# Kernel tuning notes

Hardware: AMD Instinct MI355X
Metric: run time of the kernel (lower is better)

Reference implementation:

```python
import jax, jax.numpy as jnp
import numpy as np
from jax import lax

DIM = 256
STATE = 64
D_INNER = 256          # ssd_expand=1 * dim
HIDDEN = 4 * DIM       # mlp_ratio=4
CONV_DIM = 3 * STATE
B, H, W = 16, 64, 64
EPS = 1e-5


def dwconv(x, w, b=None):
    # depthwise 3x3, SAME padding; x:(B,C,H,W) w:(C,1,3,3)
    y = lax.conv_general_dilated(x, w, (1, 1), 'SAME',
                                 feature_group_count=x.shape[1],
                                 dimension_numbers=('NCHW', 'OIHW', 'NCHW'))
    if b is not None:
        y = y + b[None, :, None, None]
    return y


def batchnorm(x, g, b):
    m = x.mean(axis=(0, 2, 3), keepdims=True)
    v = x.var(axis=(0, 2, 3), keepdims=True)
    return (x - m) * jax.lax.rsqrt(v + EPS) * g[None, :, None, None] + b[None, :, None, None]


def layernorm1d(x, w, b):
    # norm over channel dim of (B,C,L)
    m = x.mean(axis=1, keepdims=True)
    v = x.var(axis=1, keepdims=True)
    return (x - m) * jax.lax.rsqrt(v + EPS) * w[None, :, None] + b[None, :, None]


def pw1d(x, w, b):
    # 1x1 conv1d: x:(B,Cin,L), w:(Cout,Cin)
    return jnp.einsum('oc,bcl->bol', w, x) + b[None, :, None]


def setup_inputs() -> dict:
    key = jax.random.key(0)
    ks = jax.random.split(key, 16)
    s = 0.02
    inp = {
        'x': jax.random.normal(ks[0], (B, DIM, H, W), jnp.float32),
        'alpha': 1e-4 * jnp.ones((4, DIM), jnp.float32),
        'dw1_w': s * jax.random.normal(ks[1], (DIM, 1, 3, 3), jnp.float32),
        'bn1_g': jnp.ones((DIM,), jnp.float32),
        'bn1_b': jnp.zeros((DIM,), jnp.float32),
        'dw2_w': s * jax.random.normal(ks[2], (DIM, 1, 3, 3), jnp.float32),
        'bn2_g': jnp.ones((DIM,), jnp.float32),
        'bn2_b': jnp.zeros((DIM,), jnp.float32),
        'ln_w': jnp.ones((DIM,), jnp.float32),
        'ln_b': jnp.zeros((DIM,), jnp.float32),
        'bcdt_w': s * jax.random.normal(ks[3], (CONV_DIM, DIM), jnp.float32),
        'bcdt_b': jnp.zeros((CONV_DIM,), jnp.float32),
        'mdw_w': s * jax.random.normal(ks[4], (CONV_DIM, 1, 3, 3), jnp.float32),
        'mdw_b': jnp.zeros((CONV_DIM,), jnp.float32),
        'hz_w': s * jax.random.normal(ks[5], (2 * D_INNER, DIM), jnp.float32),
        'hz_b': jnp.zeros((2 * D_INNER,), jnp.float32),
        'out_w': s * jax.random.normal(ks[6], (DIM, D_INNER), jnp.float32),
        'out_b': jnp.zeros((DIM,), jnp.float32),
        'A': jax.random.uniform(ks[7], (STATE,), jnp.float32, 1.0, 16.0),
        'D': jnp.ones((1,), jnp.float32),
        'ffn_w1': s * jax.random.normal(ks[8], (HIDDEN, DIM), jnp.float32),
        'ffn_b1': jnp.zeros((HIDDEN,), jnp.float32),
        'ffn_w2': s * jax.random.normal(ks[9], (DIM, HIDDEN), jnp.float32),
        'ffn_b2': jnp.zeros((DIM,), jnp.float32),
    }
    return inp


def _mixer(xf, bcdt_w, bcdt_b, mdw_w, mdw_b, hz_w, hz_b, out_w, out_b, A, D, h_, w_):
    # xf: (B, dim, L)
    b = xf.shape[0]
    BCdt = pw1d(xf, bcdt_w, bcdt_b).reshape(b, CONV_DIM, h_, w_)
    BCdt = dwconv(BCdt, mdw_w, mdw_b).reshape(b, CONV_DIM, h_ * w_)
    Bm, Cm, dt = jnp.split(BCdt, [STATE, 2 * STATE], axis=1)  # (B,S,L) each
    Am = jax.nn.softmax(dt + A[None, :, None], axis=-1)
    AB = Am * Bm                                   # (B,S,L)
    h = jnp.einsum('bcl,bsl->bcs', xf, AB)         # (B,dim,S) small
    hz = jnp.einsum('oc,bcs->bos', hz_w, h) + hz_b[None, :, None]
    hh, z = jnp.split(hz, [D_INNER], axis=1)
    hh = hh * jax.nn.silu(z) + hh * D[0]
    hh = jnp.einsum('oc,bcs->bos', out_w, hh) + out_b[None, :, None]
    y = jnp.einsum('bcs,bsl->bcl', hh, Cm)         # (B,dim,L)
    return y.reshape(b, DIM, h_, w_)


def reference(x, alpha, dw1_w, bn1_g, bn1_b, dw2_w, bn2_g, bn2_b, ln_w, ln_b,
              bcdt_w, bcdt_b, mdw_w, mdw_b, hz_w, hz_b, out_w, out_b, A, D,
              ffn_w1, ffn_b1, ffn_w2, ffn_b2):
    a = jax.nn.sigmoid(alpha)[:, None, :, None, None]  # (4,1,dim,1,1)
    x = (1 - a[0]) * x + a[0] * batchnorm(dwconv(x, dw1_w), bn1_g, bn1_b)
    x_prev = x
    b, _, h_, w_ = x.shape
    xf = layernorm1d(x.reshape(b, DIM, h_ * w_), ln_w, ln_b)
    y = _mixer(xf, bcdt_w, bcdt_b, mdw_w, mdw_b, hz_w, hz_b, out_w, out_b, A, D, h_, w_)
    x = (1 - a[1]) * x_prev + a[1] * y
    x = (1 - a[2]) * x + a[2] * batchnorm(dwconv(x, dw2_w), bn2_g, bn2_b)
    # FFN: 1x1 conv -> GELU -> 1x1 conv
    hdn = jax.nn.gelu(jnp.einsum('oc,bchw->bohw', ffn_w1, x) + ffn_b1[None, :, None, None])
    x_ffn = jnp.einsum('oc,bchw->bohw', ffn_w2, hdn) + ffn_b2[None, :, None, None]
    x = (1 - a[3]) * x + a[3] * x_ffn
    return x
```

## Files before the change

### kernel.cpp

```cpp
#include <hip/hip_runtime.h>
#include <stdint.h>


typedef __attribute__((ext_vector_type(8))) short bf16x8;
typedef __attribute__((ext_vector_type(4))) float f32x4;

__device__ __forceinline__ unsigned short f2b(float f){
  union { float f; unsigned int u; } v; v.f = f;
  unsigned int r = v.u + 0x7FFFu + ((v.u >> 16) & 1u);
  return (unsigned short)(r >> 16);
}
__device__ __forceinline__ float b2f(unsigned short h){
  union { unsigned int u; float f; } v; v.u = ((unsigned int)h) << 16;
  return v.f;
}
__device__ __forceinline__ float sigm(float x){ return 1.0f / (1.0f + __expf(-x)); }
__device__ __forceinline__ float gelu_fast(float v){
  float t = v * (-2.3022059f - 0.10294886f * v * v);
  float e = __builtin_amdgcn_exp2f(t);
  return v * __builtin_amdgcn_rcpf(1.0f + e);
}
__device__ __forceinline__ unsigned int cvtpk(float lo, float hi){
  unsigned int r;
  asm volatile("v_cvt_pk_bf16_f32 %0, %1, %2" : "=v"(r) : "v"(lo), "v"(hi));
  return r;
}
__device__ __forceinline__ f32x4 mfma16(bf16x8 a, bf16x8 b, f32x4 c){
  return __builtin_amdgcn_mfma_f32_16x16x32_bf16(a, b, c, 0, 0, 0);
}
__device__ __forceinline__ bf16x8 ldb8g(const unsigned short* p){
  return *reinterpret_cast<const bf16x8*>(p);
}
__device__ __forceinline__ f32x4 zero4(){ f32x4 v = {0.f, 0.f, 0.f, 0.f}; return v; }
__device__ __forceinline__ void gload_lds16(const unsigned short* g, unsigned short* l){
  __builtin_amdgcn_global_load_lds(
      (const __attribute__((address_space(1))) void*)g,
      (__attribute__((address_space(3))) void*)l, 16, 0, 0);
}

__global__ __launch_bounds__(256) void k_setup(
    const float* __restrict__ w1, const float* __restrict__ w2,
    const float* __restrict__ bw, const float* __restrict__ hzw,
    const float* __restrict__ outw,
    unsigned short* __restrict__ w1b, unsigned short* __restrict__ w2b,
    unsigned short* __restrict__ bwb, unsigned short* __restrict__ hzwb,
    unsigned short* __restrict__ outwb){
  int tid = blockIdx.x * 256 + threadIdx.x;
  if (tid < 1024 * 256){ w1b[tid] = f2b(w1[tid]); w2b[tid] = f2b(w2[tid]); }
  if (tid < 192 * 256)  bwb[tid] = f2b(bw[tid]);
  if (tid < 512 * 256)  hzwb[tid] = f2b(hzw[tid]);
  if (tid < 256 * 256)  outwb[tid] = f2b(outw[tid]);
}

__global__ __launch_bounds__(256) void k_conv_stats(
    const float* __restrict__ x, const float* __restrict__ w,
    float* __restrict__ bnsum, float* __restrict__ bnsq){
  __shared__ float t[66 * 66];
  __shared__ float rs[4], rq[4];
  int bc = blockIdx.x; int c = bc & 255;
  const float* xp = x + (size_t)bc * 4096;
  int tid = threadIdx.x;
  for (int i = tid; i < 66 * 66; i += 256) t[i] = 0.f;
  __syncthreads();
  #pragma unroll
  for (int j = 0; j < 4; j++){
    int p4 = tid + j * 256;
    float4 v = reinterpret_cast<const float4*>(xp)[p4];
    int p = p4 * 4; int y = p >> 6, xx = p & 63;
    int base = (y + 1) * 66 + xx + 1;
    t[base] = v.x; t[base + 1] = v.y; t[base + 2] = v.z; t[base + 3] = v.w;
  }
  __syncthreads();
  float w0 = w[c*9+0], w1 = w[c*9+1], w2 = w[c*9+2], w3 = w[c*9+3], w4 = w[c*9+4];
  float w5 = w[c*9+5], w6 = w[c*9+6], w7 = w[c*9+7], w8 = w[c*9+8];
  float s = 0.f, q = 0.f;
  #pragma unroll
  for (int j = 0; j < 16; j++){
    int p = tid + j * 256; int y = p >> 6, xx = p & 63;
    const float* r0 = &t[y * 66 + xx];
    float v = r0[0]*w0 + r0[1]*w1 + r0[2]*w2 + r0[66]*w3 + r0[67]*w4 + r0[68]*w5
            + r0[132]*w6 + r0[133]*w7 + r0[134]*w8;
    s += v; q += v * v;
  }
  #pragma unroll
  for (int off = 32; off > 0; off >>= 1){ s += __shfl_down(s, off); q += __shfl_down(q, off); }
  if ((tid & 63) == 0){ rs[tid >> 6] = s; rq[tid >> 6] = q; }
  __syncthreads();
  if (tid == 0){
    atomicAdd(&bnsum[c], rs[0] + rs[1] + rs[2] + rs[3]);
    atomicAdd(&bnsq[c],  rq[0] + rq[1] + rq[2] + rq[3]);
  }
}

__global__ __launch_bounds__(256) void k_conv_bn_blend(
    const float* __restrict__ x, const float* __restrict__ w,
    const float* __restrict__ bnsum, const float* __restrict__ bnsq,
    const float* __restrict__ g, const float* __restrict__ bb,
    const float* __restrict__ alpha, float* __restrict__ out){
  __shared__ float t[66 * 66];
  int bc = blockIdx.x; int c = bc & 255;
  const float* xp = x + (size_t)bc * 4096;
  float* op = out + (size_t)bc * 4096;
  int tid = threadIdx.x;
  for (int i = tid; i < 66 * 66; i += 256) t[i] = 0.f;
  __syncthreads();
  #pragma unroll
  for (int j = 0; j < 4; j++){
    int p4 = tid + j * 256;
    float4 v = reinterpret_cast<const float4*>(xp)[p4];
    int p = p4 * 4; int y = p >> 6, xx = p & 63;
    int base = (y + 1) * 66 + xx + 1;
    t[base] = v.x; t[base + 1] = v.y; t[base + 2] = v.z; t[base + 3] = v.w;
  }
  __syncthreads();
  float w0 = w[c*9+0], w1 = w[c*9+1], w2 = w[c*9+2], w3 = w[c*9+3], w4 = w[c*9+4];
  float w5 = w[c*9+5], w6 = w[c*9+6], w7 = w[c*9+7], w8 = w[c*9+8];
  float m  = bnsum[c] * (1.f / 65536.f);
  float var = bnsq[c] * (1.f / 65536.f) - m * m;
  float sc = rsqrtf(var + 1e-5f) * g[c];
  float bias = bb[c];
  float a = sigm(alpha[c]);
  #pragma unroll
  for (int j = 0; j < 16; j++){
    int p = tid + j * 256; int y = p >> 6, xx = p & 63;
    const float* r0 = &t[y * 66 + xx];
    float v = r0[0]*w0 + r0[1]*w1 + r0[2]*w2 + r0[66]*w3 + r0[67]*w4 + r0[68]*w5
            + r0[132]*w6 + r0[133]*w7 + r0[134]*w8;
    float xv = t[(y + 1) * 66 + xx + 1];
    op[p] = (1.f - a) * xv + a * ((v - m) * sc + bias);
  }
}

__global__ __launch_bounds__(256) void k_ln(
    const float* __restrict__ x1, const float* __restrict__ lnw,
    const float* __restrict__ lnb, unsigned short* __restrict__ xf,
    unsigned short* __restrict__ xfT){
  __shared__ unsigned short st[256 * 65];
  __shared__ float reds[4][64], redq[4][64];
  int b = blockIdx.x >> 6, lt = blockIdx.x & 63; int l0 = lt * 64;
  int t = threadIdx.x, w = t >> 6, lane = t & 63;
  const float* xp = x1 + ((size_t)b * 256) * 4096 + l0 + lane;
  float s = 0.f, q = 0.f;
  for (int i = 0; i < 64; i++){
    int c = w * 64 + i;
    float v = xp[(size_t)c * 4096];
    s += v; q += v * v;
    st[c * 65 + lane] = f2b(v);
  }
  reds[w][lane] = s; redq[w][lane] = q;
  __syncthreads();
  s = reds[0][lane] + reds[1][lane] + reds[2][lane] + reds[3][lane];
  q = redq[0][lane] + redq[1][lane] + redq[2][lane] + redq[3][lane];
  float m = s * (1.f / 256.f);
  float r = rsqrtf(q * (1.f / 256.f) - m * m + 1e-5f);
  for (int i = 0; i < 64; i++){
    int c = w * 64 + i;
    float v = b2f(st[c * 65 + lane]);
    unsigned short h = f2b((v - m) * r * lnw[c] + lnb[c]);
    st[c * 65 + lane] = h;
    xf[((size_t)(b * 256 + c)) * 4096 + l0 + lane] = h;
  }
  __syncthreads();
  int p = t >> 4, cc = t & 15;
  for (int pi = 0; pi < 4; pi++){
    int px = p + pi * 16;
    #pragma unroll
    for (int j = 0; j < 2; j++){
      int c0 = (j * 16 + cc) * 8;
      unsigned short vv[8];
      #pragma unroll
      for (int k = 0; k < 8; k++) vv[k] = st[(c0 + k) * 65 + px];
      *reinterpret_cast<uint4*>(&xfT[((size_t)(b * 4096 + l0 + px)) * 256 + c0]) =
          *reinterpret_cast<uint4*>(vv);
    }
  }
}

__global__ __launch_bounds__(256) void k_xt(
    const float* __restrict__ x, unsigned short* __restrict__ xT){
  __shared__ unsigned short st[256 * 65];
  int b = blockIdx.x >> 6, lt = blockIdx.x & 63; int l0 = lt * 64;
  int t = threadIdx.x, w = t >> 6, lane = t & 63;
  const float* xp = x + ((size_t)b * 256) * 4096 + l0 + lane;
  for (int i = 0; i < 64; i++){
    int c = w * 64 + i;
    st[c * 65 + lane] = f2b(xp[(size_t)c * 4096]);
  }
  __syncthreads();
  int p = t >> 4, cc = t & 15;
  for (int pi = 0; pi < 4; pi++){
    int px = p + pi * 16;
    #pragma unroll
    for (int j = 0; j < 2; j++){
      int c0 = (j * 16 + cc) * 8;
      unsigned short vv[8];
      #pragma unroll
      for (int k = 0; k < 8; k++) vv[k] = st[(c0 + k) * 65 + px];
      *reinterpret_cast<uint4*>(&xT[((size_t)(b * 4096 + l0 + px)) * 256 + c0]) =
          *reinterpret_cast<uint4*>(vv);
    }
  }
}

__global__ __launch_bounds__(256) void k_bcdt(
    const unsigned short* __restrict__ xfT, const unsigned short* __restrict__ wb,
    const float* __restrict__ bias, unsigned short* __restrict__ outp){
  int blk = blockIdx.x; int b = blk >> 6, lt = blk & 63; int l0 = lt * 64;
  int t = threadIdx.x; int wv = t >> 6, lane = t & 63;
  int col = lane & 15, g = lane >> 4;
  f32x4 acc[3][4];
  #pragma unroll
  for (int mm = 0; mm < 3; mm++)
    #pragma unroll
    for (int nn = 0; nn < 4; nn++) acc[mm][nn] = zero4();
  for (int k = 0; k < 8; k++){
    bf16x8 av[3], bv[4];
    #pragma unroll
    for (int mm = 0; mm < 3; mm++){
      int o = (wv * 3 + mm) * 16 + col;
      av[mm] = ldb8g(&wb[(size_t)o * 256 + k * 32 + g * 8]);
    }
    #pragma unroll
    for (int nn = 0; nn < 4; nn++){
      int l = l0 + nn * 16 + col;
      bv[nn] = ldb8g(&xfT[((size_t)(b * 4096 + l)) * 256 + k * 32 + g * 8]);
    }
    #pragma unroll
    for (int mm = 0; mm < 3; mm++)
      #pragma unroll
      for (int nn = 0; nn < 4; nn++) acc[mm][nn] = mfma16(av[mm], bv[nn], acc[mm][nn]);
  }
  #pragma unroll
  for (int mm = 0; mm < 3; mm++)
    #pragma unroll
    for (int nn = 0; nn < 4; nn++)
      #pragma unroll
      for (int r = 0; r < 4; r++){
        int o = (wv * 3 + mm) * 16 + g * 4 + r;
        int l = l0 + nn * 16 + col;
        outp[((size_t)(b * 192 + o)) * 4096 + l] = f2b(acc[mm][nn][r] + bias[o]);
      }
}

__global__ __launch_bounds__(256) void k_conv_mid(
    const unsigned short* __restrict__ in, const float* __restrict__ w,
    const float* __restrict__ wbias, unsigned short* __restrict__ outp,
    float* __restrict__ smmax, float* __restrict__ smsum){
  __shared__ float t[66 * 66];
  __shared__ float red[8];
  int blk = blockIdx.x; int b = blk / 192, ch = blk % 192;
  const unsigned short* xp = in + (size_t)blk * 4096;
  unsigned short* op = outp + (size_t)blk * 4096;
  int tid = threadIdx.x;
  for (int i = tid; i < 66 * 66; i += 256) t[i] = 0.f;
  __syncthreads();
  #pragma unroll
  for (int j = 0; j < 2; j++){
    int p8 = tid + j * 256;
    unsigned short vv[8];
    *reinterpret_cast<uint4*>(vv) = reinterpret_cast<const uint4*>(xp)[p8];
    int p = p8 * 8; int y = p >> 6, xx = p & 63;
    int base = (y + 1) * 66 + xx + 1;
    #pragma unroll
    for (int k = 0; k < 8; k++) t[base + k] = b2f(vv[k]);
  }
  __syncthreads();
  float w0 = w[ch*9+0], w1 = w[ch*9+1], w2 = w[ch*9+2], w3 = w[ch*9+3], w4 = w[ch*9+4];
  float w5 = w[ch*9+5], w6 = w[ch*9+6], w7 = w[ch*9+7], w8 = w[ch*9+8];
  float bv = wbias[ch];
  float vloc[16];
  float mx = -1e30f;
  #pragma unroll
  for (int j = 0; j < 16; j++){
    int p = tid + j * 256; int y = p >> 6, xx = p & 63;
    const float* r0 = &t[y * 66 + xx];
    float v = r0[0]*w0 + r0[1]*w1 + r0[2]*w2 + r0[66]*w3 + r0[67]*w4 + r0[68]*w5
            + r0[132]*w6 + r0[133]*w7 + r0[134]*w8 + bv;
    unsigned short h = f2b(v);
    op[p] = h;
    float vb = b2f(h);
    vloc[j] = vb;
    mx = fmaxf(mx, vb);
  }
  if (ch >= 128){
    #pragma unroll
    for (int off = 32; off > 0; off >>= 1) mx = fmaxf(mx, __shfl_down(mx, off));
    if ((tid & 63) == 0) red[tid >> 6] = mx;
    __syncthreads();
    float M = fmaxf(fmaxf(red[0], red[1]), fmaxf(red[2], red[3]));
    float se = 0.f;
    #pragma unroll
    for (int j = 0; j < 16; j++) se += __expf(vloc[j] - M);
    #pragma unroll
    for (int off = 32; off > 0; off >>= 1) se += __shfl_down(se, off);
    if ((tid & 63) == 0) red[4 + (tid >> 6)] = se;
    __syncthreads();
    if (tid == 0){
      smmax[b * 64 + ch - 128] = M;
      smsum[b * 64 + ch - 128] = red[4] + red[5] + red[6] + red[7];
    }
  }
}

__global__ __launch_bounds__(256) void k_ab(
    const unsigned short* __restrict__ bc, const float* __restrict__ smmax,
    const float* __restrict__ smsum, unsigned short* __restrict__ ab){
  int blk = blockIdx.x; int b = blk >> 6, s = blk & 63;
  const unsigned short* dt = bc + ((size_t)(b * 192 + 128 + s)) * 4096;
  const unsigned short* bm = bc + ((size_t)(b * 192 + s)) * 4096;
  unsigned short* o = ab + ((size_t)(b * 64 + s)) * 4096;
  float M = smmax[b * 64 + s];
  float inv = 1.f / smsum[b * 64 + s];
  for (int i = threadIdx.x; i < 4096; i += 256)
    o[i] = f2b(__expf(b2f(dt[i]) - M) * inv * b2f(bm[i]));
}

__global__ __launch_bounds__(256) void k_cmt(
    const unsigned short* __restrict__ bc, unsigned short* __restrict__ cmt){
  __shared__ float t[64 * 65];
  int blk = blockIdx.x; int b = blk >> 6, lt = blk & 63; int l0 = lt * 64;
  int tid = threadIdx.x;
  #pragma unroll
  for (int it = 0; it < 2; it++){
    int row = (tid >> 3) + it * 32;
    int lq = (tid & 7) * 8;
    const unsigned short* p = bc + ((size_t)(b * 192 + 64 + row)) * 4096 + l0 + lq;
    unsigned short vv[8];
    *reinterpret_cast<uint4*>(vv) = *reinterpret_cast<const uint4*>(p);
    #pragma unroll
    for (int k = 0; k < 8; k++) t[row * 65 + lq + k] = b2f(vv[k]);
  }
  __syncthreads();
  #pragma unroll
  for (int it = 0; it < 2; it++){
    int l = (tid >> 3) + it * 32;
    int sq = (tid & 7) * 8;
    unsigned short vv[8];
    #pragma unroll
    for (int k = 0; k < 8; k++) vv[k] = f2b(t[(sq + k) * 65 + l]);
    *reinterpret_cast<uint4*>(&cmt[((size_t)(b * 4096 + l0 + l)) * 64 + sq]) =
        *reinterpret_cast<uint4*>(vv);
  }
}

__global__ __launch_bounds__(512) void k_h(
    const unsigned short* __restrict__ ab, const unsigned short* __restrict__ xf,
    float* __restrict__ hpart){
  int blk = blockIdx.x; int b = blk & 15, chunk = blk >> 4;
  int t = threadIdx.x; int wv = t >> 6, lane = t & 63;
  int col = lane & 15, g = lane >> 4;
  int mt = wv & 3, nh = wv >> 2;
  f32x4 acc[8];
  #pragma unroll
  for (int nn = 0; nn < 8; nn++) acc[nn] = zero4();
  int lbase = chunk * 256;
  const unsigned short* ap = ab + ((size_t)(b * 64 + mt * 16 + col)) * 4096 + lbase + g * 8;
  for (int ks = 0; ks < 8; ks++){
    bf16x8 av = ldb8g(ap + ks * 32);
    #pragma unroll
    for (int nn = 0; nn < 8; nn++){
      int c = nh * 128 + nn * 16 + col;
      bf16x8 bv = ldb8g(&xf[((size_t)(b * 256 + c)) * 4096 + lbase + ks * 32 + g * 8]);
      acc[nn] = mfma16(av, bv, acc[nn]);
    }
  }
  #pragma unroll
  for (int nn = 0; nn < 8; nn++)
    #pragma unroll
    for (int r = 0; r < 4; r++){
      int s = mt * 16 + g * 4 + r;
      int c = nh * 128 + nn * 16 + col;
      hpart[(((size_t)chunk * 16 + b) * 64 + s) * 256 + c] = acc[nn][r];
    }
}

__global__ __launch_bounds__(256) void k_hsum(
    const float* __restrict__ hp, unsigned short* __restrict__ hsb){
  int i = blockIdx.x * 256 + threadIdx.x;
  float s = 0.f;
  #pragma unroll
  for (int c = 0; c < 16; c++) s += hp[(size_t)c * 262144 + i];
  hsb[i] = f2b(s);
}

__global__ __launch_bounds__(256) void k_hz(
    const unsigned short* __restrict__ hsb, const unsigned short* __restrict__ hzwb,
    const float* __restrict__ hzb, const float* __restrict__ Dp,
    unsigned short* __restrict__ hh1b){
  int blk = blockIdx.x; int b = blk >> 2, og = blk & 3;
  int t = threadIdx.x, wv = t >> 6, lane = t & 63;
  int col = lane & 15, g = lane >> 4;
  int ou = og * 64 + wv * 16;
  int oz = 256 + ou;
  f32x4 au[4], az[4];
  #pragma unroll
  for (int nn = 0; nn < 4; nn++){ au[nn] = zero4(); az[nn] = zero4(); }
  const unsigned short* bbase = hsb + (size_t)b * 64 * 256;
  for (int k = 0; k < 8; k++){
    bf16x8 a_u = ldb8g(&hzwb[(size_t)(ou + col) * 256 + k * 32 + g * 8]);
    bf16x8 a_z = ldb8g(&hzwb[(size_t)(oz + col) * 256 + k * 32 + g * 8]);
    bf16x8 bv[4];
    #pragma unroll
    for (int nn = 0; nn < 4; nn++)
      bv[nn] = ldb8g(bbase + (size_t)(nn * 16 + col) * 256 + k * 32 + g * 8);
    #pragma unroll
    for (int nn = 0; nn < 4; nn++){
      au[nn] = mfma16(a_u, bv[nn], au[nn]);
      az[nn] = mfma16(a_z, bv[nn], az[nn]);
    }
  }
  float Dv = Dp[0];
  #pragma unroll
  for (int nn = 0; nn < 4; nn++){
    int s = nn * 16 + col;
    float hv[4];
    #pragma unroll
    for (int r = 0; r < 4; r++){
      int o = ou + g * 4 + r;
      float u = au[nn][r] + hzb[o];
      float z = az[nn][r] + hzb[o + 256];
      float sl = z / (1.f + __expf(-z));
      hv[r] = u * (sl + Dv);
    }
    unsigned int p0 = cvtpk(hv[0], hv[1]), p1 = cvtpk(hv[2], hv[3]);
    uint2 pv; pv.x = p0; pv.y = p1;
    *reinterpret_cast<uint2*>(&hh1b[((size_t)(b * 64 + s)) * 256 + ou + g * 4]) = pv;
  }
}

__global__ __launch_bounds__(256) void k_out(
    const unsigned short* __restrict__ hh1b, const unsigned short* __restrict__ outwb,
    const float* __restrict__ ob, unsigned short* __restrict__ hh2){
  int blk = blockIdx.x; int b = blk >> 2, dg = blk & 3;
  int t = threadIdx.x, wv = t >> 6, lane = t & 63;
  int col = lane & 15, g = lane >> 4;
  int d0 = dg * 64 + wv * 16;
  f32x4 acc[4];
  #pragma unroll
  for (int nn = 0; nn < 4; nn++) acc[nn] = zero4();
  const unsigned short* bbase = hh1b + (size_t)b * 64 * 256;
  for (int k = 0; k < 8; k++){
    bf16x8 a = ldb8g(&outwb[(size_t)(d0 + col) * 256 + k * 32 + g * 8]);
    bf16x8 bv[4];
    #pragma unroll
    for (int nn = 0; nn < 4; nn++)
      bv[nn] = ldb8g(bbase + (size_t)(nn * 16 + col) * 256 + k * 32 + g * 8);
    #pragma unroll
    for (int nn = 0; nn < 4; nn++) acc[nn] = mfma16(a, bv[nn], acc[nn]);
  }
  #pragma unroll
  for (int nn = 0; nn < 4; nn++){
    int s = nn * 16 + col;
    #pragma unroll
    for (int r = 0; r < 4; r++){
      int d = d0 + g * 4 + r;
      hh2[((size_t)(b * 256 + d)) * 64 + s] = f2b(acc[nn][r] + ob[d]);
    }
  }
}

__global__ __launch_bounds__(256) void k_y_blend(
    const unsigned short* __restrict__ hh2, const unsigned short* __restrict__ cmt,
    const float* __restrict__ alpha, float* __restrict__ x){
  int blk = blockIdx.x; int b = blk >> 6, lt = blk & 63; int l0 = lt * 64;
  int t = threadIdx.x; int wv = t >> 6, lane = t & 63;
  int col = lane & 15, g = lane >> 4;
  f32x4 acc[4][4];
  #pragma unroll
  for (int mm = 0; mm < 4; mm++)
    #pragma unroll
    for (int nn = 0; nn < 4; nn++) acc[mm][nn] = zero4();
  #pragma unroll
  for (int k = 0; k < 2; k++){
    bf16x8 av[4], bv[4];
    #pragma unroll
    for (int mm = 0; mm < 4; mm++){
      int c = (wv * 4 + mm) * 16 + col;
      av[mm] = ldb8g(&hh2[((size_t)(b * 256 + c)) * 64 + k * 32 + g * 8]);
    }
    #pragma unroll
    for (int nn = 0; nn < 4; nn++){
      int l = l0 + nn * 16 + col;
      bv[nn] = ldb8g(&cmt[((size_t)(b * 4096 + l)) * 64 + k * 32 + g * 8]);
    }
    #pragma unroll
    for (int mm = 0; mm < 4; mm++)
      #pragma unroll
      for (int nn = 0; nn < 4; nn++) acc[mm][nn] = mfma16(av[mm], bv[nn], acc[mm][nn]);
  }
  #pragma unroll
  for (int mm = 0; mm < 4; mm++)
    #pragma unroll
    for (int r = 0; r < 4; r++){
      int c = (wv * 4 + mm) * 16 + g * 4 + r;
      float a1 = sigm(alpha[c]);
      #pragma unroll
      for (int nn = 0; nn < 4; nn++){
        int l = l0 + nn * 16 + col;
        size_t idx = ((size_t)(b * 256 + c)) * 4096 + l;
        float xv = x[idx];
        x[idx] = (1.f - a1) * xv + a1 * acc[mm][nn][r];
      }
    }
}

__global__ __launch_bounds__(256, 4) void k_ffn1(
    const unsigned short* __restrict__ xT, const unsigned short* __restrict__ w1b,
    const float* __restrict__ b1, unsigned short* __restrict__ Hh, int b0){
  __shared__ unsigned short smem[17408];
  unsigned short* At = smem;
  unsigned short* Bt = smem + 8192;
  int wk = ((blockIdx.x & 7) << 8) + (blockIdx.x >> 3);
  int mt = wk & 7, nt = wk >> 3;
  int t = threadIdx.x, wv = t >> 6, lane = t & 63;
  int col = lane & 15, g = lane >> 4;
  int wr = wv >> 1, wc = wv & 1;
  const unsigned short* ag = w1b + (size_t)(mt * 128) * 256;
  const unsigned short* bg = xT + ((size_t)b0 * 4096 + (size_t)nt * 128) * 256;
  f32x4 acc[4][4];
  #pragma unroll
  for (int mm = 0; mm < 4; mm++)
    #pragma unroll
    for (int nn = 0; nn < 4; nn++) acc[mm][nn] = zero4();
  for (int kk = 0; kk < 4; kk++){
    __syncthreads();
    #pragma unroll
    for (int j = 0; j < 4; j++){
      int id = t + j * 256;
      int row = id >> 3, kc = (id & 7) * 8;
      gload_lds16(ag + (size_t)row * 256 + kk * 64 + kc, At + id * 8);
      gload_lds16(bg + (size_t)row * 256 + kk * 64 + kc, Bt + id * 8);
    }
    __syncthreads();
    #pragma unroll
    for (int ks = 0; ks < 2; ks++){
      bf16x8 av[4], bv[4];
      #pragma unroll
      for (int mm = 0; mm < 4; mm++)
        av[mm] = *reinterpret_cast<const bf16x8*>(&At[(wr * 64 + mm * 16 + col) * 64 + ks * 32 + g * 8]);
      #pragma unroll
      for (int nn = 0; nn < 4; nn++)
        bv[nn] = *reinterpret_cast<const bf16x8*>(&Bt[(wc * 64 + nn * 16 + col) * 64 + ks * 32 + g * 8]);
      #pragma unroll
      for (int mm = 0; mm < 4; mm++)
        #pragma unroll
        for (int nn = 0; nn < 4; nn++)
          acc[mm][nn] = mfma16(av[mm], bv[nn], acc[mm][nn]);
    }
  }
  __syncthreads();
  #pragma unroll
  for (int mm = 0; mm < 4; mm++){
    int o4 = wr * 64 + mm * 16 + g * 4;
    #pragma unroll
    for (int nn = 0; nn < 4; nn++){
      int lloc = wc * 64 + nn * 16 + col;
      float gv[4];
      #pragma unroll
      for (int r = 0; r < 4; r++)
        gv[r] = gelu_fast(acc[mm][nn][r] + b1[mt * 128 + o4 + r]);
      uint2 pv; pv.x = cvtpk(gv[0], gv[1]); pv.y = cvtpk(gv[2], gv[3]);
      *reinterpret_cast<uint2*>(&smem[lloc * 136 + o4]) = pv;
    }
  }
  __syncthreads();
  size_t hb = (size_t)nt * 128;
  #pragma unroll
  for (int j = 0; j < 8; j++){
    int id = t + j * 256;
    int l = id >> 4, oc = id & 15;
    uint4 v = *reinterpret_cast<const uint4*>(&smem[l * 136 + oc * 8]);
    *reinterpret_cast<uint4*>(&Hh[(hb + l) * 1024 + mt * 128 + oc * 8]) = v;
  }
}

__global__ __launch_bounds__(256, 4) void k_ffn2(
    const unsigned short* __restrict__ Hh, const unsigned short* __restrict__ w2b,
    const float* __restrict__ b2, const float* __restrict__ alpha3,
    float* __restrict__ x, int b0){
  __shared__ unsigned short smem[16384];
  unsigned short* At = smem;
  unsigned short* Bt = smem + 8192;
  int wk = ((blockIdx.x & 7) << 6) + (blockIdx.x >> 3);
  int mt = wk & 1, nt = wk >> 1;
  int t = threadIdx.x, wv = t >> 6, lane = t & 63;
  int col = lane & 15, g = lane >> 4;
  int wr = wv >> 1, wc = wv & 1;
  const unsigned short* ag = w2b + (size_t)(mt * 128) * 1024;
  const unsigned short* bg = Hh + (size_t)(nt * 128) * 1024;
  f32x4 acc[4][4];
  #pragma unroll
  for (int mm = 0; mm < 4; mm++)
    #pragma unroll
    for (int nn = 0; nn < 4; nn++) acc[mm][nn] = zero4();
  for (int kk = 0; kk < 16; kk++){
    __syncthreads();
    #pragma unroll
    for (int j = 0; j < 4; j++){
      int id = t + j * 256;
      int row = id >> 3, kc = (id & 7) * 8;
      gload_lds16(ag + (size_t)row * 1024 + kk * 64 + kc, At + id * 8);
      gload_lds16(bg + (size_t)row * 1024 + kk * 64 + kc, Bt + id * 8);
    }
    __syncthreads();
    #pragma unroll
    for (int ks = 0; ks < 2; ks++){
      bf16x8 av[4], bv[4];
      #pragma unroll
      for (int mm = 0; mm < 4; mm++)
        av[mm] = *reinterpret_cast<const bf16x8*>(&At[(wr * 64 + mm * 16 + col) * 64 + ks * 32 + g * 8]);
      #pragma unroll
      for (int nn = 0; nn < 4; nn++)
        bv[nn] = *reinterpret_cast<const bf16x8*>(&Bt[(wc * 64 + nn * 16 + col) * 64 + ks * 32 + g * 8]);
      #pragma unroll
      for (int mm = 0; mm < 4; mm++)
        #pragma unroll
        for (int nn = 0; nn < 4; nn++)
          acc[mm][nn] = mfma16(av[mm], bv[nn], acc[mm][nn]);
    }
  }
  #pragma unroll
  for (int mm = 0; mm < 4; mm++)
    #pragma unroll
    for (int r = 0; r < 4; r++){
      int d = mt * 128 + wr * 64 + mm * 16 + g * 4 + r;
      float a3 = sigm(alpha3[d]);
      float bias = b2[d];
      #pragma unroll
      for (int nn = 0; nn < 4; nn++){
        int lh = nt * 128 + wc * 64 + nn * 16 + col;
        int b = b0 + (lh >> 12);
        int l = lh & 4095;
        size_t idx = ((size_t)(b * 256 + d)) * 4096 + l;
        float xv = x[idx];
        x[idx] = (1.f - a3) * xv + a3 * (acc[mm][nn][r] + bias);
      }
    }
}

extern "C" void kernel_launch(void* const* d_in, const int* in_sizes, int n_in,
                              void* d_out, int out_size, void* d_ws, size_t ws_size,
                              hipStream_t stream){
  (void)in_sizes; (void)n_in; (void)out_size; (void)ws_size;
  const float* x      = (const float*)d_in[0];
  const float* alpha  = (const float*)d_in[1];
  const float* dw1_w  = (const float*)d_in[2];
  const float* bn1_g  = (const float*)d_in[3];
  const float* bn1_b  = (const float*)d_in[4];
  const float* dw2_w  = (const float*)d_in[5];
  const float* bn2_g  = (const float*)d_in[6];
  const float* bn2_b  = (const float*)d_in[7];
  const float* ln_w   = (const float*)d_in[8];
  const float* ln_b   = (const float*)d_in[9];
  const float* bcdt_w = (const float*)d_in[10];
  const float* bcdt_b = (const float*)d_in[11];
  const float* mdw_w  = (const float*)d_in[12];
  const float* mdw_b  = (const float*)d_in[13];
  const float* hz_w   = (const float*)d_in[14];
  const float* hz_b   = (const float*)d_in[15];
  const float* out_w  = (const float*)d_in[16];
  const float* out_b  = (const float*)d_in[17];
  const float* Dvec   = (const float*)d_in[19];
  const float* ffn_w1 = (const float*)d_in[20];
  const float* ffn_b1 = (const float*)d_in[21];
  const float* ffn_w2 = (const float*)d_in[22];
  const float* ffn_b2 = (const float*)d_in[23];
  float* out = (float*)d_out;
  char* ws = (char*)d_ws;

  const size_t OFF_BCRAW = 0;
  const size_t OFF_BCC   = 25165824;
  const size_t OFF_XF    = 50331648;
  const size_t OFF_XFT   = 83886080;
  const size_t OFF_AB    = 0;
  const size_t OFF_CMT   = 8388608;
  const size_t OFF_HPART = 16777216;
  const size_t OFF_HSB   = 83886080;
  const size_t OFF_HH1B  = 84410368;
  const size_t OFF_HH2   = 84934656;
  const size_t OFF_H     = 0;
  const size_t OFF_X3T   = 67108864;
  const size_t OFF_W1B   = 117440512;
  const size_t OFF_W2B   = 117964800;
  const size_t OFF_BWB   = 118489088;
  const size_t OFF_HZWB  = 118587392;
  const size_t OFF_OUTWB = 119111680;
  const size_t OFF_STATS = 119373824;
  const size_t OFF_SMMAX = 119377920;
  const size_t OFF_SMSUM = 119382016;

  unsigned short* bcraw = (unsigned short*)(ws + OFF_BCRAW);
  unsigned short* bcc   = (unsigned short*)(ws + OFF_BCC);
  unsigned short* xf    = (unsigned short*)(ws + OFF_XF);
  unsigned short* xfT   = (unsigned short*)(ws + OFF_XFT);
  unsigned short* ab    = (unsigned short*)(ws + OFF_AB);
  unsigned short* cmt   = (unsigned short*)(ws + OFF_CMT);
  float* hpart = (float*)(ws + OFF_HPART);
  unsigned short* hsb  = (unsigned short*)(ws + OFF_HSB);
  unsigned short* hh1b = (unsigned short*)(ws + OFF_HH1B);
  unsigned short* hh2  = (unsigned short*)(ws + OFF_HH2);
  unsigned short* Hbuf = (unsigned short*)(ws + OFF_H);
  unsigned short* x3T  = (unsigned short*)(ws + OFF_X3T);
  unsigned short* w1b = (unsigned short*)(ws + OFF_W1B);
  unsigned short* w2b = (unsigned short*)(ws + OFF_W2B);
  unsigned short* bwb = (unsigned short*)(ws + OFF_BWB);
  unsigned short* hzwb  = (unsigned short*)(ws + OFF_HZWB);
  unsigned short* outwb = (unsigned short*)(ws + OFF_OUTWB);
  float* bn1sum = (float*)(ws + OFF_STATS);
  float* bn1sq  = bn1sum + 256;
  float* bn2sum = bn1sum + 512;
  float* bn2sq  = bn1sum + 768;
  float* smmax = (float*)(ws + OFF_SMMAX);
  float* smsum = (float*)(ws + OFF_SMSUM);

  hipMemsetAsync(ws + OFF_STATS, 0, 4096, stream);
  k_setup<<<1024, 256, 0, stream>>>(ffn_w1, ffn_w2, bcdt_w, hz_w, out_w,
                                    w1b, w2b, bwb, hzwb, outwb);
  k_conv_stats<<<4096, 256, 0, stream>>>(x, dw1_w, bn1sum, bn1sq);
  k_conv_bn_blend<<<4096, 256, 0, stream>>>(x, dw1_w, bn1sum, bn1sq,
                                            bn1_g, bn1_b, alpha + 0, out);
  k_ln<<<1024, 256, 0, stream>>>(out, ln_w, ln_b, xf, xfT);
  k_bcdt<<<1024, 256, 0, stream>>>(xfT, bwb, bcdt_b, bcraw);
  k_conv_mid<<<3072, 256, 0, stream>>>(bcraw, mdw_w, mdw_b, bcc, smmax, smsum);
  k_ab<<<1024, 256, 0, stream>>>(bcc, smmax, smsum, ab);
  k_cmt<<<1024, 256, 0, stream>>>(bcc, cmt);
  k_h<<<256, 512, 0, stream>>>(ab, xf, hpart);
  k_hsum<<<1024, 256, 0, stream>>>(hpart, hsb);
  k_hz<<<64, 256, 0, stream>>>(hsb, hzwb, hz_b, Dvec, hh1b);
  k_out<<<64, 256, 0, stream>>>(hh1b, outwb, out_b, hh2);
  k_y_blend<<<1024, 256, 0, stream>>>(hh2, cmt, alpha + 256, out);
  k_conv_stats<<<4096, 256, 0, stream>>>(out, dw2_w, bn2sum, bn2sq);
  k_conv_bn_blend<<<4096, 256, 0, stream>>>(out, dw2_w, bn2sum, bn2sq,
                                            bn2_g, bn2_b, alpha + 512, out);
  k_xt<<<1024, 256, 0, stream>>>(out, x3T);
  k_ffn1<<<2048, 256, 0, stream>>>(x3T, w1b, ffn_b1, Hbuf, 0);
  k_ffn2<<<512, 256, 0, stream>>>(Hbuf, w2b, ffn_b2, alpha + 768, out, 0);
  k_ffn1<<<2048, 256, 0, stream>>>(x3T, w1b, ffn_b1, Hbuf, 8);
  k_ffn2<<<512, 256, 0, stream>>>(Hbuf, w2b, ffn_b2, alpha + 768, out, 8);
}
```

Measured before the change: 387.2 us.

## Keep FFN1 weight tile resident in LDS across N-tiles; merge ab/cmt launches

k_ffn1 now loads its full 128x256 weight slice into LDS once per block and loops over four N-tiles, streaming only the activation tile each time. This removes the repeated weight loads from global memory, and the grid shrinks from 2048 to 512 blocks. The epilogue reuses the B buffer with an XOR-swizzled layout, written in two halves. The LDS footprint grows to about 80KB and occupancy drops to 2 blocks per CU, which costs some latency hiding. Separately, k_ab and k_cmt are fused into a single 2048-block launch to save one launch.

```diff
diff --git a/kernel.cpp b/kernel.cpp
--- a/kernel.cpp
+++ b/kernel.cpp
@@ -302,23 +302,25 @@
   }
 }
 
-__global__ __launch_bounds__(256) void k_ab(
+__global__ __launch_bounds__(256) void k_ab_cmt(
     const unsigned short* __restrict__ bc, const float* __restrict__ smmax,
-    const float* __restrict__ smsum, unsigned short* __restrict__ ab){
-  int blk = blockIdx.x; int b = blk >> 6, s = blk & 63;
-  const unsigned short* dt = bc + ((size_t)(b * 192 + 128 + s)) * 4096;
-  const unsigned short* bm = bc + ((size_t)(b * 192 + s)) * 4096;
-  unsigned short* o = ab + ((size_t)(b * 64 + s)) * 4096;
-  float M = smmax[b * 64 + s];
-  float inv = 1.f / smsum[b * 64 + s];
-  for (int i = threadIdx.x; i < 4096; i += 256)
-    o[i] = f2b(__expf(b2f(dt[i]) - M) * inv * b2f(bm[i]));
-}
-
-__global__ __launch_bounds__(256) void k_cmt(
-    const unsigned short* __restrict__ bc, unsigned short* __restrict__ cmt){
+    const float* __restrict__ smsum, unsigned short* __restrict__ ab,
+    unsigned short* __restrict__ cmt){
   __shared__ float t[64 * 65];
-  int blk = blockIdx.x; int b = blk >> 6, lt = blk & 63; int l0 = lt * 64;
+  int blk = blockIdx.x;
+  if (blk < 1024){
+    int b = blk >> 6, s = blk & 63;
+    const unsigned short* dt = bc + ((size_t)(b * 192 + 128 + s)) * 4096;
+    const unsigned short* bm = bc + ((size_t)(b * 192 + s)) * 4096;
+    unsigned short* o = ab + ((size_t)(b * 64 + s)) * 4096;
+    float M = smmax[b * 64 + s];
+    float inv = 1.f / smsum[b * 64 + s];
+    for (int i = threadIdx.x; i < 4096; i += 256)
+      o[i] = f2b(__expf(b2f(dt[i]) - M) * inv * b2f(bm[i]));
+    return;
+  }
+  blk -= 1024;
+  int b = blk >> 6, lt = blk & 63; int l0 = lt * 64;
   int tid = threadIdx.x;
   #pragma unroll
   for (int it = 0; it < 2; it++){
@@ -504,73 +506,102 @@
     }
 }
 
-__global__ __launch_bounds__(256, 4) void k_ffn1(
+__global__ __launch_bounds__(256, 2) void k_ffn1(
     const unsigned short* __restrict__ xT, const unsigned short* __restrict__ w1b,
     const float* __restrict__ b1, unsigned short* __restrict__ Hh, int b0){
-  __shared__ unsigned short smem[17408];
-  unsigned short* At = smem;
-  unsigned short* Bt = smem + 8192;
-  int wk = ((blockIdx.x & 7) << 8) + (blockIdx.x >> 3);
-  int mt = wk & 7, nt = wk >> 3;
+  __shared__ unsigned short Asm[128 * 256];
+  __shared__ unsigned short Bsm[128 * 64];
+  int xcd = blockIdx.x & 7;
+  int j   = blockIdx.x >> 3;
+  int mt  = j & 7, grp = j >> 3;
   int t = threadIdx.x, wv = t >> 6, lane = t & 63;
   int col = lane & 15, g = lane >> 4;
   int wr = wv >> 1, wc = wv & 1;
-  const unsigned short* ag = w1b + (size_t)(mt * 128) * 256;
-  const unsigned short* bg = xT + ((size_t)b0 * 4096 + (size_t)nt * 128) * 256;
-  f32x4 acc[4][4];
+  {
+    const unsigned short* ag = w1b + (size_t)(mt * 128) * 256;
+    #pragma unroll
+    for (int it = 0; it < 16; it++){
+      int id = t + it * 256;
+      int row = id >> 5, kc = (id & 31) * 8;
+      gload_lds16(ag + (size_t)row * 256 + kc, Asm + id * 8);
+    }
+  }
+  float bias[4][4];
   #pragma unroll
   for (int mm = 0; mm < 4; mm++)
     #pragma unroll
-    for (int nn = 0; nn < 4; nn++) acc[mm][nn] = zero4();
-  for (int kk = 0; kk < 4; kk++){
-    __syncthreads();
-    #pragma unroll
-    for (int j = 0; j < 4; j++){
-      int id = t + j * 256;
-      int row = id >> 3, kc = (id & 7) * 8;
-      gload_lds16(ag + (size_t)row * 256 + kk * 64 + kc, At + id * 8);
-      gload_lds16(bg + (size_t)row * 256 + kk * 64 + kc, Bt + id * 8);
-    }
-    __syncthreads();
-    #pragma unroll
-    for (int ks = 0; ks < 2; ks++){
-      bf16x8 av[4], bv[4];
-      #pragma unroll
-      for (int mm = 0; mm < 4; mm++)
-        av[mm] = *reinterpret_cast<const bf16x8*>(&At[(wr * 64 + mm * 16 + col) * 64 + ks * 32 + g * 8]);
-      #pragma unroll
-      for (int nn = 0; nn < 4; nn++)
-        bv[nn] = *reinterpret_cast<const bf16x8*>(&Bt[(wc * 64 + nn * 16 + col) * 64 + ks * 32 + g * 8]);
-      #pragma unroll
-      for (int mm = 0; mm < 4; mm++)
+    for (int r = 0; r < 4; r++)
+      bias[mm][r] = b1[mt * 128 + wr * 64 + mm * 16 + g * 4 + r];
+  for (int i = 0; i < 4; i++){
+    int nt = xcd * 32 + grp * 4 + i;
+    const unsigned short* bg = xT + ((size_t)b0 * 4096 + (size_t)nt * 128) * 256;
+    f32x4 acc[4][4];
+    #pragma unroll
+    for (int mm = 0; mm < 4; mm++)
+      #pragma unroll
+      for (int nn = 0; nn < 4; nn++) acc[mm][nn] = zero4();
+    for (int kk = 0; kk < 4; kk++){
+      __syncthreads();
+      #pragma unroll
+      for (int it2 = 0; it2 < 4; it2++){
+        int id = t + it2 * 256;
+        int row = id >> 3, kc = (id & 7) * 8;
+        gload_lds16(bg + (size_t)row * 256 + kk * 64 + kc, Bsm + id * 8);
+      }
+      __syncthreads();
+      #pragma unroll
+      for (int ks = 0; ks < 2; ks++){
+        bf16x8 av[4], bv[4];
+        #pragma unroll
+        for (int mm = 0; mm < 4; mm++)
+          av[mm] = *reinterpret_cast<const bf16x8*>(
+              &Asm[(wr * 64 + mm * 16 + col) * 256 + kk * 64 + ks * 32 + g * 8]);
         #pragma unroll
         for (int nn = 0; nn < 4; nn++)
-          acc[mm][nn] = mfma16(av[mm], bv[nn], acc[mm][nn]);
-    }
-  }
-  __syncthreads();
-  #pragma unroll
-  for (int mm = 0; mm < 4; mm++){
-    int o4 = wr * 64 + mm * 16 + g * 4;
-    #pragma unroll
-    for (int nn = 0; nn < 4; nn++){
-      int lloc = wc * 64 + nn * 16 + col;
-      float gv[4];
-      #pragma unroll
-      for (int r = 0; r < 4; r++)
-        gv[r] = gelu_fast(acc[mm][nn][r] + b1[mt * 128 + o4 + r]);
-      uint2 pv; pv.x = cvtpk(gv[0], gv[1]); pv.y = cvtpk(gv[2], gv[3]);
-      *reinterpret_cast<uint2*>(&smem[lloc * 136 + o4]) = pv;
-    }
-  }
-  __syncthreads();
-  size_t hb = (size_t)nt * 128;
-  #pragma unroll
-  for (int j = 0; j < 8; j++){
-    int id = t + j * 256;
-    int l = id >> 4, oc = id & 15;
-    uint4 v = *reinterpret_cast<const uint4*>(&smem[l * 136 + oc * 8]);
-    *reinterpret_cast<uint4*>(&Hh[(hb + l) * 1024 + mt * 128 + oc * 8]) = v;
+          bv[nn] = *reinterpret_cast<const bf16x8*>(
+              &Bsm[(wc * 64 + nn * 16 + col) * 64 + ks * 32 + g * 8]);
+        #pragma unroll
+        for (int mm = 0; mm < 4; mm++)
+          #pragma unroll
+          for (int nn = 0; nn < 4; nn++)
+            acc[mm][nn] = mfma16(av[mm], bv[nn], acc[mm][nn]);
+      }
+    }
+    __syncthreads();
+    char* bb8 = (char*)Bsm;
+    #pragma unroll
+    for (int h = 0; h < 2; h++){
+      if (wc == h){
+        #pragma unroll
+        for (int mm = 0; mm < 4; mm++){
+          int o4 = wr * 64 + mm * 16 + g * 4;
+          #pragma unroll
+          for (int nn = 0; nn < 4; nn++){
+            int l = nn * 16 + col;
+            float gv[4];
+            #pragma unroll
+            for (int r = 0; r < 4; r++)
+              gv[r] = gelu_fast(acc[mm][nn][r] + bias[mm][r]);
+            uint2 pv; pv.x = cvtpk(gv[0], gv[1]); pv.y = cvtpk(gv[2], gv[3]);
+            int byte = ((l * 128 + o4) * 2) ^ ((l & 7) << 4);
+            *reinterpret_cast<uint2*>(bb8 + byte) = pv;
+          }
+        }
+      }
+      __syncthreads();
+      {
+        int row = t >> 2, oc = t & 3;
+        size_t hrow = ((size_t)nt * 128 + h * 64 + row) * 1024
+                    + (size_t)mt * 128 + oc * 32;
+        #pragma unroll
+        for (int u = 0; u < 4; u++){
+          int byte = (row * 256 + oc * 64 + u * 16) ^ ((row & 7) << 4);
+          *reinterpret_cast<uint4*>(&Hh[hrow + u * 8]) =
+              *reinterpret_cast<const uint4*>(bb8 + byte);
+        }
+      }
+      __syncthreads();
+    }
   }
 }
 
@@ -722,8 +753,7 @@
   k_ln<<<1024, 256, 0, stream>>>(out, ln_w, ln_b, xf, xfT);
   k_bcdt<<<1024, 256, 0, stream>>>(xfT, bwb, bcdt_b, bcraw);
   k_conv_mid<<<3072, 256, 0, stream>>>(bcraw, mdw_w, mdw_b, bcc, smmax, smsum);
-  k_ab<<<1024, 256, 0, stream>>>(bcc, smmax, smsum, ab);
-  k_cmt<<<1024, 256, 0, stream>>>(bcc, cmt);
+  k_ab_cmt<<<2048, 256, 0, stream>>>(bcc, smmax, smsum, ab, cmt);
   k_h<<<256, 512, 0, stream>>>(ab, xf, hpart);
   k_hsum<<<1024, 256, 0, stream>>>(hpart, hsb);
   k_hz<<<64, 256, 0, stream>>>(hsb, hzwb, hz_b, Dvec, hh1b);
@@ -733,8 +763,8 @@
   k_conv_bn_blend<<<4096, 256, 0, stream>>>(out, dw2_w, bn2sum, bn2sq,
                                             bn2_g, bn2_b, alpha + 512, out);
   k_xt<<<1024, 256, 0, stream>>>(out, x3T);
-  k_ffn1<<<2048, 256, 0, stream>>>(x3T, w1b, ffn_b1, Hbuf, 0);
+  k_ffn1<<<512, 256, 0, stream>>>(x3T, w1b, ffn_b1, Hbuf, 0);
   k_ffn2<<<512, 256, 0, stream>>>(Hbuf, w2b, ffn_b2, alpha + 768, out, 0);
-  k_ffn1<<<2048, 256, 0, stream>>>(x3T, w1b, ffn_b1, Hbuf, 8);
+  k_ffn1<<<512, 256, 0, stream>>>(x3T, w1b, ffn_b1, Hbuf, 8);
   k_ffn2<<<512, 256, 0, stream>>>(Hbuf, w2b, ffn_b2, alpha + 768, out, 8);
 }
```

New measurement: 423.2 us. 1.09x slower.
